# Optimization experiments

Hardware: AMD Instinct MI355X
Metric: run time of the kernel (lower is better)

Reference implementation:

```python
import jax, jax.numpy as jnp
import numpy as np

E, T, D, DFF = 8, 16384, 512, 2048  # experts, tokens, d_model, d_ff
ROUTE_P = 0.25  # ~ top_k=2 of E=8


def setup_inputs() -> dict:
    key = jax.random.key(0)
    k_x, k_m, k_w1, k_w2 = jax.random.split(key, 4)
    x = jax.random.normal(k_x, (T, D), dtype=jnp.float32)
    mask = jax.random.bernoulli(k_m, ROUTE_P, (E, T))  # bool [E, T]
    W1 = jax.random.normal(k_w1, (E, D, DFF), dtype=jnp.float32) * (1.0 / np.sqrt(D).astype(np.float32))
    b1 = jnp.zeros((E, DFF), dtype=jnp.float32)
    W2 = jax.random.normal(k_w2, (E, DFF, D), dtype=jnp.float32) * (1.0 / np.sqrt(DFF).astype(np.float32))
    b2 = jnp.zeros((E, D), dtype=jnp.float32)
    return {"x": x, "W1": W1, "b1": b1, "W2": W2, "b2": b2, "mask": mask}


def reference(x, W1, b1, W2, b2, mask):
    # vmapped per-expert FFN on shared tokens; mask zeroes non-routed tokens.
    # h: [E, T, DFF]
    h = jax.nn.gelu(jnp.einsum('td,edf->etf', x, W1) + b1[:, None, :])
    # y: [E, T, D]
    y = jnp.einsum('etf,efd->etd', h, W2) + b2[:, None, :]
    return jnp.where(mask[:, :, None], y, jnp.zeros((), dtype=y.dtype))
```

## Files before the change

kernel.cpp:

```cpp
#include <hip/hip_runtime.h>
#include <hip/hip_bf16.h>

#define NE 8
#define NT 16384
#define ND 512
#define NF 2048
#define BT 64

typedef __attribute__((ext_vector_type(8))) short bf16x8;
typedef __attribute__((ext_vector_type(4))) float f32x4;
typedef unsigned short u16;

#define WAITV(n) asm volatile("s_waitcnt vmcnt(" #n ")" ::: "memory")

__device__ __forceinline__ u16 f2bf(float f) {
  union { float f; unsigned u; } c; c.f = f;
  unsigned u = c.u;
  return (u16)((u + 0x7FFFu + ((u >> 16) & 1u)) >> 16);
}

__device__ __forceinline__ float gelu_tanh(float x) {
  float z = 0.7978845608028654f * (x + 0.044715f * x * x * x);
  float e = __expf(2.0f * z);
  float th = 1.0f - 2.0f * __builtin_amdgcn_rcpf(e + 1.0f);
  return 0.5f * x * (1.0f + th);
}

__device__ __forceinline__ void gl_lds16(const void* g, void* l) {
  __builtin_amdgcn_global_load_lds(
      (const __attribute__((address_space(1))) unsigned int*)g,
      (__attribute__((address_space(3))) unsigned int*)l, 16, 0, 0);
}

template<int MODE>
__global__ void pack_w(const float* __restrict__ in, u16* __restrict__ outp) {
  constexpr int K = MODE ? 2048 : 512;
  constexpr int R = MODE ? 512 : 2048;
  __shared__ float tile[32][33];
  int e = blockIdx.z, bx = blockIdx.x, by = blockIdx.y;
  int k0 = bx * 32, r0 = by * 32;
  int tx = threadIdx.x & 31, ty = threadIdx.x >> 5;
  const float* ip = in + ((size_t)e * K + k0) * R + r0;
  #pragma unroll
  for (int i = 0; i < 4; i++)
    tile[ty + i * 8][tx] = ip[(size_t)(ty + i * 8) * R + tx];
  __syncthreads();
  size_t base; int rowb;
  if (MODE == 0) { base = (((size_t)e * 8 + (by >> 3)) * 16 + bx) * 8192; rowb = (by & 7) * 32; }
  else           { base = (((size_t)e * 8 + (bx >> 3)) * 8 + (bx & 7)) * 16384; rowb = by * 32; }
  int row = rowb + tx;
  int byo = row * 64 + ((ty * 8) ^ (((row >> 1) & 3) << 4));
  union { u16 s[4]; ushort4 v; } o;
  #pragma unroll
  for (int j = 0; j < 4; j++) o.s[j] = f2bf(tile[ty * 4 + j][tx]);
  *(ushort4*)((char*)outp + base * 2 + byo) = o.v;
}

__global__ void x_to_bf16(const float* __restrict__ x, u16* __restrict__ xbf) {
  int i = blockIdx.x * 256 + threadIdx.x;
  float4 v = ((const float4*)x)[i];
  union { u16 s[4]; unsigned long long ll; } o;
  o.s[0] = f2bf(v.x); o.s[1] = f2bf(v.y); o.s[2] = f2bf(v.z); o.s[3] = f2bf(v.w);
  ((unsigned long long*)xbf)[i] = o.ll;
}

__global__ void compact_mask(const int* __restrict__ mask, int* __restrict__ idx,
                             int* __restrict__ counts) {
  int e = blockIdx.x;
  __shared__ int wsum[4];
  __shared__ int base;
  if (threadIdx.x == 0) base = 0;
  const int* m = mask + (size_t)e * NT;
  int lane = threadIdx.x & 63, w = threadIdx.x >> 6;
  for (int c0 = 0; c0 < NT; c0 += 256) {
    __syncthreads();
    int i = c0 + threadIdx.x;
    int mi = (m[i] != 0);
    unsigned long long b = __ballot(mi);
    if (lane == 0) wsum[w] = __popcll(b);
    __syncthreads();
    int off = base;
    for (int ww = 0; ww < w; ww++) off += wsum[ww];
    off += __popcll(b & ((1ull << lane) - 1ull));
    if (mi) idx[(size_t)e * NT + off] = i;
    __syncthreads();
    if (threadIdx.x == 0) base += wsum[0] + wsum[1] + wsum[2] + wsum[3];
  }
  __syncthreads();
  if (threadIdx.x == 0) counts[e] = base;
}

__launch_bounds__(512, 2)
__global__ void moe_ffn(const u16* __restrict__ xbf, const u16* __restrict__ W1p,
                        const float* __restrict__ b1f, const u16* __restrict__ W2p,
                        const float* __restrict__ b2f,
                        const int* __restrict__ idx, const int* __restrict__ counts,
                        float* __restrict__ out) {
  int e = blockIdx.y;
  int cnt = counts[e];
  int r0 = blockIdx.x * BT;
  if (r0 >= cnt) return;
  int rem = cnt - r0; if (rem > BT) rem = BT;

  __shared__ __align__(16) u16 arena[3 * 16384];
  __shared__ __align__(16) u16 hs[BT * 256];
  __shared__ __align__(16) float b1s[NF];
  __shared__ __align__(16) float b2s[ND];
  __shared__ int ids_s[BT];

  int tid = threadIdx.x, lane = tid & 63, w = tid >> 6;
  int wm = w & 1, wn = w >> 1;
  int l15 = lane & 15, l4 = lane >> 4;

  if (tid < BT) ids_s[tid] = idx[(size_t)e * NT + r0 + ((tid < rem) ? tid : 0)];
  __syncthreads();

  int q = w & 3;
  int xrow = q * 16 + (lane >> 2);
  size_t xsrc = (size_t)ids_s[xrow] * (ND * 2) +
                (((lane & 3) * 16) ^ (((xrow >> 1) & 3) << 4));
  const char* xbyte = (const char*)xbf;

  int aoff[2], boff1[4], hbase[2], hswz[2], boff2[8];
  #pragma unroll
  for (int g = 0; g < 2; g++) {
    int row = wm * 32 + g * 16 + l15;
    aoff[g] = 16384 + row * 64 + ((l4 * 16) ^ (((row >> 1) & 3) << 4));
    hbase[g] = row * 512; hswz[g] = (row & 7) << 4;
  }
  #pragma unroll
  for (int h = 0; h < 4; h++) {
    int row = wn * 64 + h * 16 + l15;
    boff1[h] = row * 64 + ((l4 * 16) ^ (((row >> 1) & 3) << 4));
  }
  #pragma unroll
  for (int h = 0; h < 8; h++) {
    int row = wn * 128 + h * 16 + l15;
    boff2[h] = row * 64 + ((l4 * 16) ^ (((row >> 1) & 3) << 4));
  }

  const char* w1b = (const char*)W1p + (size_t)e * (8 * 16 * 16384);
  const char* w2b = (const char*)W2p + (size_t)e * (8 * 8 * 32768);

  auto STAGE1 = [&](int c, int kb, int s) {
    const char* pb = w1b + ((size_t)c * 16 + kb) * 16384;
    char* lb = (char*)arena + s * 32768;
    gl_lds16(pb + (w * 2 + 0) * 1024 + lane * 16, lb + (w * 2 + 0) * 1024);
    gl_lds16(pb + (w * 2 + 1) * 1024 + lane * 16, lb + (w * 2 + 1) * 1024);
    if (w < 4) gl_lds16(xbyte + xsrc + kb * 64, lb + 16384 + q * 1024);
  };
  auto STAGE2 = [&](int c, int kb, int s) {
    const char* pb = w2b + ((size_t)c * 8 + kb) * 32768;
    char* lb = (char*)arena + s * 32768;
    #pragma unroll
    for (int j = 0; j < 4; j++)
      gl_lds16(pb + (w * 4 + j) * 1024 + lane * 16, lb + (w * 4 + j) * 1024);
  };

  gl_lds16((const char*)(b1f + (size_t)e * NF) + w * 1024, (char*)b1s + w * 1024);
  if (w < 2) gl_lds16((const char*)(b2f + (size_t)e * ND) + w * 1024, (char*)b2s + w * 1024);
  STAGE1(0, 0, 0);
  STAGE1(0, 1, 1);

  f32x4 yacc[2][8];
  #pragma unroll
  for (int g = 0; g < 2; g++)
    #pragma unroll
    for (int h = 0; h < 8; h++) yacc[g][h] = (f32x4)(0.0f);

  for (int c = 0; c < 8; ++c) {
    f32x4 acc1[2][4];
    #pragma unroll
    for (int g = 0; g < 2; g++)
      #pragma unroll
      for (int h = 0; h < 4; h++) acc1[g][h] = (f32x4)(0.0f);

    for (int kb = 0; kb < 16; ++kb) {
      int s = kb % 3;
      if (kb == 15) WAITV(0);
      else if (w < 4) WAITV(3);
      else WAITV(2);
      __builtin_amdgcn_s_barrier();
      if (kb < 14) STAGE1(c, kb + 2, (kb + 2) % 3);
      else if (kb == 15) { STAGE2(c, 0, 1); STAGE2(c, 1, 2); }
      const char* lb = (const char*)arena + s * 32768;
      bf16x8 a[2], b[4];
      #pragma unroll
      for (int g = 0; g < 2; g++) a[g] = *(const bf16x8*)(lb + aoff[g]);
      #pragma unroll
      for (int h = 0; h < 4; h++) b[h] = *(const bf16x8*)(lb + boff1[h]);
      #pragma unroll
      for (int g = 0; g < 2; g++)
        #pragma unroll
        for (int h = 0; h < 4; h++)
          acc1[g][h] = __builtin_amdgcn_mfma_f32_16x16x32_bf16(a[g], b[h], acc1[g][h], 0, 0, 0);
    }

    #pragma unroll
    for (int g = 0; g < 2; g++)
      #pragma unroll
      for (int h = 0; h < 4; h++) {
        int col = wn * 64 + h * 16 + l15;
        float bb = b1s[c * 256 + col];
        #pragma unroll
        for (int j = 0; j < 4; j++) {
          int row = wm * 32 + g * 16 + l4 * 4 + j;
          float v = acc1[g][h][j] + bb;
          int byo = row * 512 + ((col * 2) ^ ((row & 7) << 4));
          *(u16*)((char*)hs + byo) = f2bf(gelu_tanh(v));
        }
      }
    asm volatile("s_waitcnt lgkmcnt(0)" ::: "memory");
    __builtin_amdgcn_s_barrier();

    for (int kb = 0; kb < 8; ++kb) {
      int s = (1 + kb) % 3;
      if (kb == 7) WAITV(0);
      else WAITV(4);
      __builtin_amdgcn_s_barrier();
      if (kb < 6) STAGE2(c, kb + 2, (1 + kb + 2) % 3);
      else if (kb == 7 && c < 7) { STAGE1(c + 1, 0, 0); STAGE1(c + 1, 1, 1); }
      const char* lb = (const char*)arena + s * 32768;
      bf16x8 a[2], b[8];
      #pragma unroll
      for (int g = 0; g < 2; g++)
        a[g] = *(const bf16x8*)((const char*)hs + hbase[g] + ((kb * 64 + l4 * 16) ^ hswz[g]));
      #pragma unroll
      for (int h = 0; h < 8; h++) b[h] = *(const bf16x8*)(lb + boff2[h]);
      #pragma unroll
      for (int g = 0; g < 2; g++)
        #pragma unroll
        for (int h = 0; h < 8; h++)
          yacc[g][h] = __builtin_amdgcn_mfma_f32_16x16x32_bf16(a[g], b[h], yacc[g][h], 0, 0, 0);
    }
  }

  #pragma unroll
  for (int g = 0; g < 2; g++)
    #pragma unroll
    for (int j = 0; j < 4; j++) {
      int row = wm * 32 + g * 16 + l4 * 4 + j;
      if (row < rem) {
        int tok = ids_s[row];
        float* orow = out + ((size_t)e * NT + tok) * ND;
        #pragma unroll
        for (int h = 0; h < 8; h++) {
          int col = wn * 128 + h * 16 + l15;
          orow[col] = yacc[g][h][j] + b2s[col];
        }
      }
    }
}

extern "C" void kernel_launch(void* const* d_in, const int* in_sizes, int n_in,
                              void* d_out, int out_size, void* d_ws, size_t ws_size,
                              hipStream_t stream) {
  const float* x  = (const float*)d_in[0];
  const float* W1 = (const float*)d_in[1];
  const float* b1 = (const float*)d_in[2];
  const float* W2 = (const float*)d_in[3];
  const float* b2 = (const float*)d_in[4];
  const int* mask = (const int*)d_in[5];

  char* ws = (char*)d_ws;
  int* counts = (int*)ws;
  int* idx    = (int*)(ws + 1024);
  u16* W1p    = (u16*)(ws + 1024 + (size_t)NE * NT * 4);
  u16* W2p    = W1p + (size_t)NE * NF * ND;
  u16* xbf    = W2p + (size_t)NE * ND * NF;

  hipMemsetAsync(d_out, 0, (size_t)out_size * sizeof(float), stream);
  pack_w<0><<<dim3(16, 64, NE), dim3(256), 0, stream>>>(W1, W1p);
  pack_w<1><<<dim3(64, 16, NE), dim3(256), 0, stream>>>(W2, W2p);
  x_to_bf16<<<dim3(NT * ND / 4 / 256), dim3(256), 0, stream>>>(x, xbf);
  compact_mask<<<dim3(NE), dim3(256), 0, stream>>>(mask, idx, counts);
  moe_ffn<<<dim3(NT / BT, NE), dim3(512), 0, stream>>>(xbf, W1p, b1, W2p, b2, idx, counts,
                                                       (float*)d_out);
}
```

Before: 429.7 us.

## Double token tile, swap MFMA operand roles, zero only unmasked rows, faster GELU

```diff
diff --git a/kernel.cpp b/kernel.cpp
--- a/kernel.cpp
+++ b/kernel.cpp
@@ -5,11 +5,12 @@
 #define NT 16384
 #define ND 512
 #define NF 2048
-#define BT 64
+#define BT 128
 
 typedef __attribute__((ext_vector_type(8))) short bf16x8;
 typedef __attribute__((ext_vector_type(4))) float f32x4;
 typedef unsigned short u16;
+typedef unsigned long long u64;
 
 #define WAITV(n) asm volatile("s_waitcnt vmcnt(" #n ")" ::: "memory")
 
@@ -19,11 +20,12 @@
   return (u16)((u + 0x7FFFu + ((u >> 16) & 1u)) >> 16);
 }
 
-__device__ __forceinline__ float gelu_tanh(float x) {
-  float z = 0.7978845608028654f * (x + 0.044715f * x * x * x);
-  float e = __expf(2.0f * z);
-  float th = 1.0f - 2.0f * __builtin_amdgcn_rcpf(e + 1.0f);
-  return 0.5f * x * (1.0f + th);
+__device__ __forceinline__ float gelu_fast(float x) {
+  float x2 = x * x;
+  float zp = x * __builtin_fmaf(0.10294325f, x2, 2.3022084f);
+  float u = __builtin_amdgcn_exp2f(zp);
+  float r = __builtin_amdgcn_rcpf(u + 1.0f);
+  return x * (1.0f - r);
 }
 
 __device__ __forceinline__ void gl_lds16(const void* g, void* l) {
@@ -59,9 +61,15 @@
 __global__ void x_to_bf16(const float* __restrict__ x, u16* __restrict__ xbf) {
   int i = blockIdx.x * 256 + threadIdx.x;
   float4 v = ((const float4*)x)[i];
-  union { u16 s[4]; unsigned long long ll; } o;
+  union { u16 s[4]; u64 ll; } o;
   o.s[0] = f2bf(v.x); o.s[1] = f2bf(v.y); o.s[2] = f2bf(v.z); o.s[3] = f2bf(v.w);
-  ((unsigned long long*)xbf)[i] = o.ll;
+  ((u64*)xbf)[i] = o.ll;
+}
+
+__global__ void zero_unmasked(const int* __restrict__ mask, float4* __restrict__ out4) {
+  int row = blockIdx.x * 2 + (threadIdx.x >> 7);
+  if (mask[row]) return;
+  out4[(size_t)row * 128 + (threadIdx.x & 127)] = float4{0.f, 0.f, 0.f, 0.f};
 }
 
 __global__ void compact_mask(const int* __restrict__ mask, int* __restrict__ idx,
@@ -96,160 +104,157 @@
                         const float* __restrict__ b2f,
                         const int* __restrict__ idx, const int* __restrict__ counts,
                         float* __restrict__ out) {
-  int e = blockIdx.y;
-  int cnt = counts[e];
-  int r0 = blockIdx.x * BT;
-  if (r0 >= cnt) return;
-  int rem = cnt - r0; if (rem > BT) rem = BT;
-
-  __shared__ __align__(16) u16 arena[3 * 16384];
+  int e = blockIdx.x & 7;
+  int r0 = (blockIdx.x >> 3) << 7;
+  if (r0 >= counts[e]) return;
+  int rem = counts[e] - r0; if (rem > BT) rem = BT;
+
+  __shared__ __align__(16) u16 arena[2 * 16384];
+  __shared__ __align__(16) u16 xp[2 * 4096];
   __shared__ __align__(16) u16 hs[BT * 256];
   __shared__ __align__(16) float b1s[NF];
   __shared__ __align__(16) float b2s[ND];
   __shared__ int ids_s[BT];
 
   int tid = threadIdx.x, lane = tid & 63, w = tid >> 6;
-  int wm = w & 1, wn = w >> 1;
+  int wt = w & 1, wfd = w >> 1;
   int l15 = lane & 15, l4 = lane >> 4;
 
   if (tid < BT) ids_s[tid] = idx[(size_t)e * NT + r0 + ((tid < rem) ? tid : 0)];
   __syncthreads();
 
-  int q = w & 3;
-  int xrow = q * 16 + (lane >> 2);
+  const char* xbyte = (const char*)xbf;
+  int xrow = w * 16 + (lane >> 2);
   size_t xsrc = (size_t)ids_s[xrow] * (ND * 2) +
                 (((lane & 3) * 16) ^ (((xrow >> 1) & 3) << 4));
-  const char* xbyte = (const char*)xbf;
-
-  int aoff[2], boff1[4], hbase[2], hswz[2], boff2[8];
-  #pragma unroll
-  for (int g = 0; g < 2; g++) {
-    int row = wm * 32 + g * 16 + l15;
-    aoff[g] = 16384 + row * 64 + ((l4 * 16) ^ (((row >> 1) & 3) << 4));
-    hbase[g] = row * 512; hswz[g] = (row & 7) << 4;
-  }
-  #pragma unroll
-  for (int h = 0; h < 4; h++) {
-    int row = wn * 64 + h * 16 + l15;
-    boff1[h] = row * 64 + ((l4 * 16) ^ (((row >> 1) & 3) << 4));
-  }
-  #pragma unroll
-  for (int h = 0; h < 8; h++) {
-    int row = wn * 128 + h * 16 + l15;
-    boff2[h] = row * 64 + ((l4 * 16) ^ (((row >> 1) & 3) << 4));
+
+  int aoff1[4], boffx[4], aoff2[8], tbase[4], tswz[4];
+  #pragma unroll
+  for (int i = 0; i < 4; i++) {
+    int rf = wfd * 64 + i * 16 + l15;
+    aoff1[i] = rf * 64 + ((l4 * 16) ^ (((rf >> 1) & 3) << 4));
+    int t = wt * 64 + i * 16 + l15;
+    boffx[i] = t * 64 + ((l4 * 16) ^ (((t >> 1) & 3) << 4));
+    tbase[i] = t * 512; tswz[i] = (t & 7) << 4;
+  }
+  #pragma unroll
+  for (int i = 0; i < 8; i++) {
+    int rd = wfd * 128 + i * 16 + l15;
+    aoff2[i] = rd * 64 + ((l4 * 16) ^ (((rd >> 1) & 3) << 4));
   }
 
   const char* w1b = (const char*)W1p + (size_t)e * (8 * 16 * 16384);
   const char* w2b = (const char*)W2p + (size_t)e * (8 * 8 * 32768);
+  char* arenaB = (char*)arena;
+  char* xpB = (char*)xp;
+  char* hsB = (char*)hs;
 
   auto STAGE1 = [&](int c, int kb, int s) {
-    const char* pb = w1b + ((size_t)c * 16 + kb) * 16384;
-    char* lb = (char*)arena + s * 32768;
-    gl_lds16(pb + (w * 2 + 0) * 1024 + lane * 16, lb + (w * 2 + 0) * 1024);
-    gl_lds16(pb + (w * 2 + 1) * 1024 + lane * 16, lb + (w * 2 + 1) * 1024);
-    if (w < 4) gl_lds16(xbyte + xsrc + kb * 64, lb + 16384 + q * 1024);
+    const char* pb = w1b + (((size_t)c * 16 + kb) << 14);
+    char* lb = arenaB + s * 32768 + w * 2048;
+    gl_lds16(pb + w * 2048 + lane * 16, lb);
+    gl_lds16(pb + w * 2048 + 1024 + lane * 16, lb + 1024);
+    gl_lds16(xbyte + xsrc + kb * 64, xpB + s * 8192 + w * 1024);
   };
   auto STAGE2 = [&](int c, int kb, int s) {
-    const char* pb = w2b + ((size_t)c * 8 + kb) * 32768;
-    char* lb = (char*)arena + s * 32768;
+    const char* pb = w2b + (((size_t)c * 8 + kb) << 15);
+    char* lb = arenaB + s * 32768 + w * 4096;
     #pragma unroll
     for (int j = 0; j < 4; j++)
-      gl_lds16(pb + (w * 4 + j) * 1024 + lane * 16, lb + (w * 4 + j) * 1024);
+      gl_lds16(pb + w * 4096 + j * 1024 + lane * 16, lb + j * 1024);
   };
 
   gl_lds16((const char*)(b1f + (size_t)e * NF) + w * 1024, (char*)b1s + w * 1024);
   if (w < 2) gl_lds16((const char*)(b2f + (size_t)e * ND) + w * 1024, (char*)b2s + w * 1024);
   STAGE1(0, 0, 0);
-  STAGE1(0, 1, 1);
-
-  f32x4 yacc[2][8];
-  #pragma unroll
-  for (int g = 0; g < 2; g++)
-    #pragma unroll
-    for (int h = 0; h < 8; h++) yacc[g][h] = (f32x4)(0.0f);
+
+  f32x4 yacc[8][4];
+  #pragma unroll
+  for (int i = 0; i < 8; i++)
+    #pragma unroll
+    for (int t = 0; t < 4; t++) yacc[i][t] = (f32x4)(0.0f);
 
   for (int c = 0; c < 8; ++c) {
-    f32x4 acc1[2][4];
-    #pragma unroll
-    for (int g = 0; g < 2; g++)
-      #pragma unroll
-      for (int h = 0; h < 4; h++) acc1[g][h] = (f32x4)(0.0f);
+    f32x4 acc1[4][4];
+    #pragma unroll
+    for (int i = 0; i < 4; i++)
+      #pragma unroll
+      for (int t = 0; t < 4; t++) acc1[i][t] = (f32x4)(0.0f);
 
     for (int kb = 0; kb < 16; ++kb) {
-      int s = kb % 3;
-      if (kb == 15) WAITV(0);
-      else if (w < 4) WAITV(3);
-      else WAITV(2);
-      __builtin_amdgcn_s_barrier();
-      if (kb < 14) STAGE1(c, kb + 2, (kb + 2) % 3);
-      else if (kb == 15) { STAGE2(c, 0, 1); STAGE2(c, 1, 2); }
-      const char* lb = (const char*)arena + s * 32768;
-      bf16x8 a[2], b[4];
-      #pragma unroll
-      for (int g = 0; g < 2; g++) a[g] = *(const bf16x8*)(lb + aoff[g]);
-      #pragma unroll
-      for (int h = 0; h < 4; h++) b[h] = *(const bf16x8*)(lb + boff1[h]);
-      #pragma unroll
-      for (int g = 0; g < 2; g++)
-        #pragma unroll
-        for (int h = 0; h < 4; h++)
-          acc1[g][h] = __builtin_amdgcn_mfma_f32_16x16x32_bf16(a[g], b[h], acc1[g][h], 0, 0, 0);
-    }
-
-    #pragma unroll
-    for (int g = 0; g < 2; g++)
-      #pragma unroll
-      for (int h = 0; h < 4; h++) {
-        int col = wn * 64 + h * 16 + l15;
-        float bb = b1s[c * 256 + col];
-        #pragma unroll
-        for (int j = 0; j < 4; j++) {
-          int row = wm * 32 + g * 16 + l4 * 4 + j;
-          float v = acc1[g][h][j] + bb;
-          int byo = row * 512 + ((col * 2) ^ ((row & 7) << 4));
-          *(u16*)((char*)hs + byo) = f2bf(gelu_tanh(v));
-        }
+      int s = kb & 1;
+      __builtin_amdgcn_s_barrier();
+      if (kb < 15) { STAGE1(c, kb + 1, s ^ 1); WAITV(3); }
+      else         { STAGE2(c, 0, 0);          WAITV(4); }
+      __builtin_amdgcn_s_barrier();
+      const char* lb = arenaB + s * 32768;
+      const char* lx = xpB + s * 8192;
+      bf16x8 a[4], b[4];
+      #pragma unroll
+      for (int i = 0; i < 4; i++) a[i] = *(const bf16x8*)(lb + aoff1[i]);
+      #pragma unroll
+      for (int t = 0; t < 4; t++) b[t] = *(const bf16x8*)(lx + boffx[t]);
+      #pragma unroll
+      for (int i = 0; i < 4; i++)
+        #pragma unroll
+        for (int t = 0; t < 4; t++)
+          acc1[i][t] = __builtin_amdgcn_mfma_f32_16x16x32_bf16(a[i], b[t], acc1[i][t], 0, 0, 0);
+    }
+
+    #pragma unroll
+    for (int i = 0; i < 4; i++) {
+      int fb = wfd * 64 + i * 16 + l4 * 4;
+      f32x4 bv = *(const f32x4*)(b1s + c * 256 + fb);
+      #pragma unroll
+      for (int t = 0; t < 4; t++) {
+        union { u16 s[4]; u64 ll; } pk;
+        #pragma unroll
+        for (int j = 0; j < 4; j++)
+          pk.s[j] = f2bf(gelu_fast(acc1[i][t][j] + bv[j]));
+        *(u64*)(hsB + tbase[t] + ((fb * 2) ^ tswz[t])) = pk.ll;
       }
+    }
     asm volatile("s_waitcnt lgkmcnt(0)" ::: "memory");
     __builtin_amdgcn_s_barrier();
 
     for (int kb = 0; kb < 8; ++kb) {
-      int s = (1 + kb) % 3;
-      if (kb == 7) WAITV(0);
-      else WAITV(4);
-      __builtin_amdgcn_s_barrier();
-      if (kb < 6) STAGE2(c, kb + 2, (1 + kb + 2) % 3);
-      else if (kb == 7 && c < 7) { STAGE1(c + 1, 0, 0); STAGE1(c + 1, 1, 1); }
-      const char* lb = (const char*)arena + s * 32768;
-      bf16x8 a[2], b[8];
-      #pragma unroll
-      for (int g = 0; g < 2; g++)
-        a[g] = *(const bf16x8*)((const char*)hs + hbase[g] + ((kb * 64 + l4 * 16) ^ hswz[g]));
-      #pragma unroll
-      for (int h = 0; h < 8; h++) b[h] = *(const bf16x8*)(lb + boff2[h]);
-      #pragma unroll
-      for (int g = 0; g < 2; g++)
-        #pragma unroll
-        for (int h = 0; h < 8; h++)
-          yacc[g][h] = __builtin_amdgcn_mfma_f32_16x16x32_bf16(a[g], b[h], yacc[g][h], 0, 0, 0);
-    }
-  }
-
-  #pragma unroll
-  for (int g = 0; g < 2; g++)
-    #pragma unroll
-    for (int j = 0; j < 4; j++) {
-      int row = wm * 32 + g * 16 + l4 * 4 + j;
-      if (row < rem) {
-        int tok = ids_s[row];
-        float* orow = out + ((size_t)e * NT + tok) * ND;
-        #pragma unroll
-        for (int h = 0; h < 8; h++) {
-          int col = wn * 128 + h * 16 + l15;
-          orow[col] = yacc[g][h][j] + b2s[col];
-        }
+      int s = kb & 1;
+      __builtin_amdgcn_s_barrier();
+      if (kb < 7)      { STAGE2(c, kb + 1, s ^ 1); WAITV(4); }
+      else if (c < 7)  { STAGE1(c + 1, 0, 0);      WAITV(3); }
+      else             { WAITV(0); }
+      __builtin_amdgcn_s_barrier();
+      const char* lb = arenaB + s * 32768;
+      bf16x8 a[8], b[4];
+      #pragma unroll
+      for (int i = 0; i < 8; i++) a[i] = *(const bf16x8*)(lb + aoff2[i]);
+      #pragma unroll
+      for (int t = 0; t < 4; t++)
+        b[t] = *(const bf16x8*)(hsB + tbase[t] + ((kb * 64 + l4 * 16) ^ tswz[t]));
+      #pragma unroll
+      for (int i = 0; i < 8; i++)
+        #pragma unroll
+        for (int t = 0; t < 4; t++)
+          yacc[i][t] = __builtin_amdgcn_mfma_f32_16x16x32_bf16(a[i], b[t], yacc[i][t], 0, 0, 0);
+    }
+  }
+
+  #pragma unroll
+  for (int i = 0; i < 8; i++) {
+    int db = wfd * 128 + i * 16 + l4 * 4;
+    f32x4 b2v = *(const f32x4*)(b2s + db);
+    #pragma unroll
+    for (int t = 0; t < 4; t++) {
+      int tt = wt * 64 + t * 16 + l15;
+      if (tt < rem) {
+        int tok = ids_s[tt];
+        f32x4 v;
+        #pragma unroll
+        for (int j = 0; j < 4; j++) v[j] = yacc[i][t][j] + b2v[j];
+        *(f32x4*)(out + ((size_t)e * NT + tok) * ND + db) = v;
       }
     }
+  }
 }
 
 extern "C" void kernel_launch(void* const* d_in, const int* in_sizes, int n_in,
@@ -269,11 +274,11 @@
   u16* W2p    = W1p + (size_t)NE * NF * ND;
   u16* xbf    = W2p + (size_t)NE * ND * NF;
 
-  hipMemsetAsync(d_out, 0, (size_t)out_size * sizeof(float), stream);
+  zero_unmasked<<<dim3(NE * NT / 2), dim3(256), 0, stream>>>(mask, (float4*)d_out);
   pack_w<0><<<dim3(16, 64, NE), dim3(256), 0, stream>>>(W1, W1p);
   pack_w<1><<<dim3(64, 16, NE), dim3(256), 0, stream>>>(W2, W2p);
   x_to_bf16<<<dim3(NT * ND / 4 / 256), dim3(256), 0, stream>>>(x, xbf);
   compact_mask<<<dim3(NE), dim3(256), 0, stream>>>(mask, idx, counts);
-  moe_ffn<<<dim3(NT / BT, NE), dim3(512), 0, stream>>>(xbf, W1p, b1, W2p, b2, idx, counts,
-                                                       (float*)d_out);
-}
+  moe_ffn<<<dim3(2048), dim3(512), 0, stream>>>(xbf, W1p, b1, W2p, b2, idx, counts,
+                                                (float*)d_out);
+}
```

Result: slower. 664.9 us (+54.7%).
